# Performance work log

Hardware: AMD Instinct MI355X
Metric: run time of the kernel (lower is better)

## Reference

```python
import jax, jax.numpy as jnp
import numpy as np
import math

D_MODEL = 1024
NHEADS = 16
HEAD_DIM = D_MODEL // NHEADS
SEQLEN = 2048
BS = 4


def setup_inputs() -> dict:
    key = jax.random.key(0)
    kq, kk, kv, kwq, kwk, kwv, kwo = jax.random.split(key, 7)
    q = jax.random.normal(kq, (SEQLEN, BS, D_MODEL), dtype=jnp.float32)
    k = jax.random.normal(kk, (SEQLEN, BS, D_MODEL), dtype=jnp.float32)
    v = jax.random.normal(kv, (SEQLEN, BS, D_MODEL), dtype=jnp.float32)
    # proper RoPE table: (seq, head_dim//2, 2) with (cos, sin)
    inv_freq = 1.0 / (10000.0 ** (np.arange(0, HEAD_DIM, 2, dtype=np.float32) / HEAD_DIM))
    angles = np.arange(SEQLEN, dtype=np.float32)[:, None] * inv_freq[None, :]
    freqs_cis = jnp.asarray(np.stack([np.cos(angles), np.sin(angles)], axis=-1))
    scale = 1.0 / math.sqrt(D_MODEL)
    wq = jax.random.normal(kwq, (D_MODEL, D_MODEL), dtype=jnp.float32) * scale
    wk = jax.random.normal(kwk, (D_MODEL, D_MODEL), dtype=jnp.float32) * scale
    wv = jax.random.normal(kwv, (D_MODEL, D_MODEL), dtype=jnp.float32) * scale
    wo = jax.random.normal(kwo, (D_MODEL, D_MODEL), dtype=jnp.float32) * scale
    return {"q": q, "k": k, "v": v, "freqs_cis": freqs_cis,
            "wq": wq, "wk": wk, "wv": wv, "wo": wo}


def _apply_rope(x, fc):
    # x: (L, B, H, hd) -> complex rotation on (hd//2, 2) pairs
    L, B, H, hd = x.shape
    x2 = x.reshape(L, B, H, hd // 2, 2)
    fc = fc[:L].reshape(L, 1, 1, hd // 2, 2)  # broadcast over batch, heads
    real = x2[..., 0] * fc[..., 0] - x2[..., 1] * fc[..., 1]
    imag = x2[..., 1] * fc[..., 0] + x2[..., 0] * fc[..., 1]
    return jnp.stack([real, imag], axis=-1).reshape(L, B, H, hd)


def reference(q, k, v, freqs_cis, wq, wk, wv, wo):
    S, B, D = q.shape
    L = k.shape[0]
    H, hd = NHEADS, HEAD_DIM
    # torch Linear: y = x @ W^T, W: (out, in)
    xq = jnp.einsum('sbd,ed->sbe', q, wq).reshape(S, B, H, hd)
    xk = jnp.einsum('lbd,ed->lbe', k, wk).reshape(L, B, H, hd)
    xv = jnp.einsum('lbd,ed->lbe', v, wv).reshape(L, B, H, hd)
    xq = _apply_rope(xq, freqs_cis)
    xk = _apply_rope(xk, freqs_cis)
    # scores: (B, H, S, L)
    scores = jnp.einsum('sbhd,lbhd->bhsl', xq, xk) / math.sqrt(hd)
    probs = jax.nn.softmax(scores.astype(jnp.float32), axis=-1).astype(xq.dtype)
    out = jnp.einsum('bhsl,lbhd->sbhd', probs, xv).reshape(S, B, H * hd)
    return jnp.einsum('sbe,de->sbd', out, wo)
```

## Files before the change

### kernel.cpp

```cpp
#include <hip/hip_runtime.h>
#include <hip/hip_bf16.h>

#define S_LEN   2048
#define BATCH   4
#define DMODEL  1024
#define NHEADS  16
#define HDIM    64
#define MROWS   (S_LEN * BATCH)

#define NE_ 8388608u
#define WE_ 1048576u

typedef unsigned int uint32;
typedef __attribute__((ext_vector_type(8))) short bf16x8;
typedef __attribute__((ext_vector_type(4))) float f32x4;

__device__ __forceinline__ ushort f2bf(float f) {
    uint32 u = __float_as_uint(f);
    uint32 r = (u + 0x7FFFu + ((u >> 16) & 1u)) >> 16;
    return (ushort)r;
}

__device__ __forceinline__ uint32 pk_bf16(float a, float b) {
    uint32 r;
    asm("v_cvt_pk_bf16_f32 %0, %1, %2" : "=v"(r) : "v"(a), "v"(b));
    return r;
}

__device__ __forceinline__ float exp2_asm(float x) {
    float r;
    asm("v_exp_f32 %0, %1" : "=v"(r) : "v"(x));
    return r;
}

__device__ __forceinline__ void gl16(const ushort* g, ushort* l) {
    __builtin_amdgcn_global_load_lds(
        (const __attribute__((address_space(1))) unsigned int*)g,
        (__attribute__((address_space(3))) unsigned int*)l,
        16, 0, 0);
}

__global__ __launch_bounds__(256) void cvt_all(const float* __restrict__ q,
                                               const float* __restrict__ k,
                                               const float* __restrict__ v,
                                               const float* __restrict__ wq,
                                               const float* __restrict__ wk,
                                               const float* __restrict__ wv,
                                               const float* __restrict__ wo,
                                               ushort* __restrict__ ws) {
    int i = blockIdx.x * 256 + threadIdx.x;
    const float* src;
    ushort* dst;
    int j;
    if (i < 3 * 2097152) {
        int t = i >> 21;
        j = i & 2097151;
        src = (t == 0) ? q : (t == 1) ? k : v;
        dst = ws + (size_t)t * NE_;
    } else {
        int u2 = i - 3 * 2097152;
        int t = u2 >> 18;
        j = u2 & 262143;
        src = (t == 0) ? wq : (t == 1) ? wk : (t == 2) ? wv : wo;
        dst = ws + 3 * (size_t)NE_ + (size_t)t * WE_;
    }
    float4 f = ((const float4*)src)[j];
    ushort4 u;
    u.x = f2bf(f.x); u.y = f2bf(f.y); u.z = f2bf(f.z); u.w = f2bf(f.w);
    ((ushort4*)dst)[j] = u;
}

__global__ __launch_bounds__(256) void qk_gemm(const ushort* __restrict__ qb,
                                               const ushort* __restrict__ kb,
                                               const ushort* __restrict__ wqb,
                                               const ushort* __restrict__ wkb,
                                               const float* __restrict__ FC,
                                               ushort* __restrict__ Qh,
                                               ushort* __restrict__ Kh) {
    __shared__ __align__(16) ushort A_lds[128 * 32];
    __shared__ __align__(16) ushort B_lds[128 * 32];

    const int tid  = threadIdx.x;
    const int lane = tid & 63;
    const int wvx  = tid >> 6;
    const int wm   = wvx >> 1, wn = wvx & 1;
    const int quad = lane >> 4, l16 = lane & 15;
    const int pid   = blockIdx.x >> 9;
    const int local = blockIdx.x & 511;
    const int m0 = (local >> 3) * 128;
    const int n0 = (local & 7) * 128;

    const ushort* A = pid ? kb : qb;
    const ushort* W = pid ? wkb : wqb;
    ushort* outb    = pid ? Kh : Qh;
    const float osc = pid ? 1.0f : 0.18033688011111793f;

    const int srow = tid >> 2;
    const int scol = (tid & 3) * 8;

    f32x4 acc[4][4] = {};

    for (int k0 = 0; k0 < 1024; k0 += 32) {
        __syncthreads();
        gl16(&A[(size_t)(m0 + srow) * 1024 + k0 + scol],      &A_lds[tid * 8]);
        gl16(&A[(size_t)(m0 + 64 + srow) * 1024 + k0 + scol], &A_lds[2048 + tid * 8]);
        gl16(&W[(size_t)(n0 + srow) * 1024 + k0 + scol],      &B_lds[tid * 8]);
        gl16(&W[(size_t)(n0 + 64 + srow) * 1024 + k0 + scol], &B_lds[2048 + tid * 8]);
        __syncthreads();

        const ushort* Ab = &A_lds[(wm * 64 + l16) * 32 + quad * 8];
        const ushort* Bb = &B_lds[(wn * 64 + l16) * 32 + quad * 8];
        bf16x8 af[4], bfr[4];
#pragma unroll
        for (int i = 0; i < 4; ++i) af[i]  = *(const bf16x8*)(Ab + i * 512);
#pragma unroll
        for (int i = 0; i < 4; ++i) bfr[i] = *(const bf16x8*)(Bb + i * 512);
#pragma unroll
        for (int im = 0; im < 4; ++im)
#pragma unroll
            for (int in = 0; in < 4; ++in)
                acc[im][in] = __builtin_amdgcn_mfma_f32_16x16x32_bf16(
                    af[im], bfr[in], acc[im][in], 0, 0, 0);
    }

#pragma unroll
    for (int im = 0; im < 4; ++im) {
        int mbase = m0 + wm * 64 + im * 16 + quad * 4;
        int s = mbase >> 2;
#pragma unroll
        for (int in = 0; in < 4; ++in) {
            int e = n0 + wn * 64 + in * 16 + l16;
            int h = e >> 6, dd = e & 63;
            float2 cs = *(const float2*)&FC[s * 64 + (dd & ~1)];
            float sgn = (dd & 1) ? 1.0f : -1.0f;
#pragma unroll
            for (int rr = 0; rr < 4; ++rr) {
                float vv = acc[im][in][rr];
                float pp = __shfl_xor(vv, 1, 64);
                float ov = (vv * cs.x + sgn * pp * cs.y) * osc;
                outb[((size_t)(rr * NHEADS + h) * S_LEN + s) * HDIM + dd] = f2bf(ov);
            }
        }
    }
}

__global__ __launch_bounds__(256) void v_gemm(const ushort* __restrict__ vb,
                                              const ushort* __restrict__ wvb,
                                              ushort* __restrict__ Vt) {
    __shared__ __align__(16) ushort A_lds[128 * 32];
    __shared__ __align__(16) ushort B_lds[128 * 32];

    const int tid  = threadIdx.x;
    const int lane = tid & 63;
    const int wvx  = tid >> 6;
    const int wm   = wvx >> 1, wn = wvx & 1;
    const int quad = lane >> 4, l16 = lane & 15;
    const int m0 = (blockIdx.x >> 3) * 128;
    const int n0 = (blockIdx.x & 7) * 128;

    const int srow = tid >> 2;
    const int scol = (tid & 3) * 8;

    f32x4 acc[4][4] = {};

    for (int k0 = 0; k0 < 1024; k0 += 32) {
        __syncthreads();
        gl16(&vb[(size_t)(m0 + srow) * 1024 + k0 + scol],      &A_lds[tid * 8]);
        gl16(&vb[(size_t)(m0 + 64 + srow) * 1024 + k0 + scol], &A_lds[2048 + tid * 8]);
        gl16(&wvb[(size_t)(n0 + srow) * 1024 + k0 + scol],      &B_lds[tid * 8]);
        gl16(&wvb[(size_t)(n0 + 64 + srow) * 1024 + k0 + scol], &B_lds[2048 + tid * 8]);
        __syncthreads();

        const ushort* Ab = &A_lds[(wm * 64 + l16) * 32 + quad * 8];
        const ushort* Bb = &B_lds[(wn * 64 + l16) * 32 + quad * 8];
        bf16x8 af[4], bfr[4];
#pragma unroll
        for (int i = 0; i < 4; ++i) af[i]  = *(const bf16x8*)(Ab + i * 512);
#pragma unroll
        for (int i = 0; i < 4; ++i) bfr[i] = *(const bf16x8*)(Bb + i * 512);
#pragma unroll
        for (int im = 0; im < 4; ++im)
#pragma unroll
            for (int in = 0; in < 4; ++in)
                acc[im][in] = __builtin_amdgcn_mfma_f32_16x16x32_bf16(
                    af[im], bfr[in], acc[im][in], 0, 0, 0);
    }

#pragma unroll
    for (int im = 0; im < 4; ++im) {
        int mbase = m0 + wm * 64 + im * 16 + quad * 4;
        int s = mbase >> 2;
        int nt2 = (s >> 4) & 3;
        int qd  = (s >> 2) & 3;
        int r2  = s & 3;
        int pos = (s & ~63) | ((nt2 >> 1) << 5) | (qd << 3) | ((nt2 & 1) << 2) | r2;
#pragma unroll
        for (int in = 0; in < 4; ++in) {
            int e = n0 + wn * 64 + in * 16 + l16;
            int h = e >> 6, dd = e & 63;
#pragma unroll
            for (int rr = 0; rr < 4; ++rr) {
                Vt[((size_t)(rr * NHEADS + h) * HDIM + dd) * S_LEN + pos] =
                    f2bf(acc[im][in][rr]);
            }
        }
    }
}

__global__ __launch_bounds__(256) void out_gemm(const ushort* __restrict__ A,
                                                const ushort* __restrict__ W,
                                                float* __restrict__ outf) {
    __shared__ __align__(16) ushort A_lds[128 * 32];
    __shared__ __align__(16) ushort B_lds[128 * 32];

    const int tid  = threadIdx.x;
    const int lane = tid & 63;
    const int wvx  = tid >> 6;
    const int wm   = wvx >> 1, wn = wvx & 1;
    const int quad = lane >> 4, l16 = lane & 15;
    const int m0 = (blockIdx.x >> 3) * 128;
    const int n0 = (blockIdx.x & 7) * 128;

    const int srow = tid >> 2;
    const int scol = (tid & 3) * 8;

    f32x4 acc[4][4] = {};

    for (int k0 = 0; k0 < 1024; k0 += 32) {
        __syncthreads();
        gl16(&A[(size_t)(m0 + srow) * 1024 + k0 + scol],      &A_lds[tid * 8]);
        gl16(&A[(size_t)(m0 + 64 + srow) * 1024 + k0 + scol], &A_lds[2048 + tid * 8]);
        gl16(&W[(size_t)(n0 + srow) * 1024 + k0 + scol],      &B_lds[tid * 8]);
        gl16(&W[(size_t)(n0 + 64 + srow) * 1024 + k0 + scol], &B_lds[2048 + tid * 8]);
        __syncthreads();

        const ushort* Ab = &A_lds[(wm * 64 + l16) * 32 + quad * 8];
        const ushort* Bb = &B_lds[(wn * 64 + l16) * 32 + quad * 8];
        bf16x8 af[4], bfr[4];
#pragma unroll
        for (int i = 0; i < 4; ++i) af[i]  = *(const bf16x8*)(Ab + i * 512);
#pragma unroll
        for (int i = 0; i < 4; ++i) bfr[i] = *(const bf16x8*)(Bb + i * 512);
#pragma unroll
        for (int im = 0; im < 4; ++im)
#pragma unroll
            for (int in = 0; in < 4; ++in)
                acc[im][in] = __builtin_amdgcn_mfma_f32_16x16x32_bf16(
                    af[im], bfr[in], acc[im][in], 0, 0, 0);
    }

#pragma unroll
    for (int im = 0; im < 4; ++im) {
        int mbase = m0 + wm * 64 + im * 16 + quad * 4;
#pragma unroll
        for (int in = 0; in < 4; ++in) {
            int e = n0 + wn * 64 + in * 16 + l16;
#pragma unroll
            for (int rr = 0; rr < 4; ++rr)
                outf[(size_t)(mbase + rr) * 1024 + e] = acc[im][in][rr];
        }
    }
}

__global__ __launch_bounds__(256) void attn_mfma(const ushort* __restrict__ Qb,
                                                 const ushort* __restrict__ Kb,
                                                 const ushort* __restrict__ Vt,
                                                 ushort* __restrict__ Ob) {
    __shared__ __align__(16) ushort KV[8192];

    const int tid  = threadIdx.x;
    const int lane = tid & 63;
    const int wv   = tid >> 6;
    const int quad = lane >> 4;
    const int l16  = lane & 15;
    const int head = blockIdx.x >> 4;
    const int qt   = blockIdx.x & 15;
    const int q0   = qt * 128 + wv * 32;
    const size_t hb = (size_t)head * (S_LEN * HDIM);

    bf16x8 qf[2][2];
#pragma unroll
    for (int im = 0; im < 2; ++im)
#pragma unroll
        for (int kk = 0; kk < 2; ++kk)
            qf[im][kk] = *(const bf16x8*)
                &Qb[hb + (size_t)(q0 + im * 16 + l16) * HDIM + kk * 32 + quad * 8];

    f32x4 o[2][4] = {};
    float lsum[2] = {0.f, 0.f};

    const int srow = tid >> 3;
    const int scol = (((tid & 7) ^ (srow & 7)) * 8);
    const int sx   = (l16 & 7) * 8;

    for (int kc = 0; kc < S_LEN; kc += 64) {
        __syncthreads();
        gl16(&Kb[hb + (size_t)(kc + srow) * HDIM + scol],      &KV[tid * 8]);
        gl16(&Kb[hb + (size_t)(kc + 32 + srow) * HDIM + scol], &KV[2048 + tid * 8]);
        gl16(&Vt[hb + (size_t)srow * S_LEN + kc + scol],        &KV[4096 + tid * 8]);
        gl16(&Vt[hb + (size_t)(32 + srow) * S_LEN + kc + scol], &KV[4096 + 2048 + tid * 8]);
        __syncthreads();

        f32x4 st[2][4] = {};
#pragma unroll
        for (int nt = 0; nt < 4; ++nt) {
            bf16x8 kf0 = *(const bf16x8*)&KV[(nt * 16 + l16) * 64 + ((quad * 8) ^ sx)];
            bf16x8 kf1 = *(const bf16x8*)&KV[(nt * 16 + l16) * 64 + ((32 + quad * 8) ^ sx)];
#pragma unroll
            for (int im = 0; im < 2; ++im) {
                st[im][nt] = __builtin_amdgcn_mfma_f32_16x16x32_bf16(
                    kf0, qf[im][0], st[im][nt], 0, 0, 0);
                st[im][nt] = __builtin_amdgcn_mfma_f32_16x16x32_bf16(
                    kf1, qf[im][1], st[im][nt], 0, 0, 0);
            }
        }

        union { uint32 d[16]; bf16x8 v[4]; } P;
#pragma unroll
        for (int im = 0; im < 2; ++im) {
            float ls = 0.f;
#pragma unroll
            for (int nt = 0; nt < 4; ++nt) {
                float p0 = exp2_asm(st[im][nt][0]);
                float p1 = exp2_asm(st[im][nt][1]);
                float p2 = exp2_asm(st[im][nt][2]);
                float p3 = exp2_asm(st[im][nt][3]);
                ls += (p0 + p1) + (p2 + p3);
                P.d[im * 8 + nt * 2]     = pk_bf16(p0, p1);
                P.d[im * 8 + nt * 2 + 1] = pk_bf16(p2, p3);
            }
            lsum[im] += ls;
        }

#pragma unroll
        for (int dt = 0; dt < 4; ++dt) {
            bf16x8 vf0 = *(const bf16x8*)&KV[4096 + (dt * 16 + l16) * 64 + ((quad * 8) ^ sx)];
            bf16x8 vf1 = *(const bf16x8*)&KV[4096 + (dt * 16 + l16) * 64 + ((32 + quad * 8) ^ sx)];
#pragma unroll
            for (int im = 0; im < 2; ++im) {
                o[im][dt] = __builtin_amdgcn_mfma_f32_16x16x32_bf16(
                    vf0, P.v[im * 2], o[im][dt], 0, 0, 0);
                o[im][dt] = __builtin_amdgcn_mfma_f32_16x16x32_bf16(
                    vf1, P.v[im * 2 + 1], o[im][dt], 0, 0, 0);
            }
        }
    }

#pragma unroll
    for (int im = 0; im < 2; ++im) {
        lsum[im] += __shfl_xor(lsum[im], 16, 64);
        lsum[im] += __shfl_xor(lsum[im], 32, 64);
    }

    __syncthreads();
    ushort* Est = &KV[wv * 2048];
#pragma unroll
    for (int im = 0; im < 2; ++im) {
        float inv = 1.0f / lsum[im];
#pragma unroll
        for (int dt = 0; dt < 4; ++dt) {
            uint2 w;
            w.x = pk_bf16(o[im][dt][0] * inv, o[im][dt][1] * inv);
            w.y = pk_bf16(o[im][dt][2] * inv, o[im][dt][3] * inv);
            *(uint2*)&Est[(im * 16 + l16) * 64 + dt * 16 + quad * 4] = w;
        }
    }
    __syncthreads();

    const int row  = lane >> 1, half = lane & 1;
    const int b = head >> 4, h = head & 15;
    const size_t ob = (size_t)((q0 + row) * BATCH + b) * 1024 + h * 64 + half * 32;
#pragma unroll
    for (int e = 0; e < 4; ++e) {
        bf16x8 t = *(const bf16x8*)&Est[row * 64 + half * 32 + e * 8];
        *(bf16x8*)&Ob[ob + e * 8] = t;
    }
}

extern "C" void kernel_launch(void* const* d_in, const int* in_sizes, int n_in,
                              void* d_out, int out_size, void* d_ws, size_t ws_size,
                              hipStream_t stream) {
    const float* q   = (const float*)d_in[0];
    const float* k   = (const float*)d_in[1];
    const float* v   = (const float*)d_in[2];
    const float* fc  = (const float*)d_in[3];
    const float* wq  = (const float*)d_in[4];
    const float* wk  = (const float*)d_in[5];
    const float* wvp = (const float*)d_in[6];
    const float* wo  = (const float*)d_in[7];

    ushort* ws = (ushort*)d_ws;
    ushort* qb  = ws;
    ushort* kb  = ws + NE_;
    ushort* vb  = ws + 2 * (size_t)NE_;
    ushort* wqb = ws + 3 * (size_t)NE_;
    ushort* wkb = wqb + WE_;
    ushort* wvb = wqb + 2 * (size_t)WE_;
    ushort* wob = wqb + 3 * (size_t)WE_;

    ushort* Qh = (ushort*)d_out;
    ushort* Kh = Qh + NE_;
    ushort* Vt = ws;
    ushort* R3 = ws + NE_;

    cvt_all<<<28672, 256, 0, stream>>>(q, k, v, wq, wk, wvp, wo, ws);

    qk_gemm<<<1024, 256, 0, stream>>>(qb, kb, wqb, wkb, fc, Qh, Kh);

    v_gemm<<<512, 256, 0, stream>>>(vb, wvb, Vt);

    attn_mfma<<<1024, 256, 0, stream>>>(Qh, Kh, Vt, R3);

    out_gemm<<<512, 256, 0, stream>>>(R3, wob, (float*)d_out);
}
```

Measured before the change: 378.0 us.

## Double-buffer K/V tiles in attention with 128-key prefetch and MFMA priority

The attention kernel now loads K and V in 128-key tiles into two LDS buffers, prefetching the next tile while the current one is computed. This removes one of the two barriers per step and hides global-load latency behind the MFMA work. The MFMA sections are also wrapped in s_setprio to favour matrix issue. In exchange, LDS per block grows from 16 KB to 64 KB, which can lower occupancy and reduce latency hiding across blocks.

```diff
diff --git a/kernel.cpp b/kernel.cpp
--- a/kernel.cpp
+++ b/kernel.cpp
@@ -266,7 +266,7 @@
                                                  const ushort* __restrict__ Kb,
                                                  const ushort* __restrict__ Vt,
                                                  ushort* __restrict__ Ob) {
-    __shared__ __align__(16) ushort KV[8192];
+    __shared__ __align__(16) ushort KV[32768];
 
     const int tid  = threadIdx.x;
     const int lane = tid & 63;
@@ -293,57 +293,89 @@
     const int scol = (((tid & 7) ^ (srow & 7)) * 8);
     const int sx   = (l16 & 7) * 8;
 
-    for (int kc = 0; kc < S_LEN; kc += 64) {
-        __syncthreads();
-        gl16(&Kb[hb + (size_t)(kc + srow) * HDIM + scol],      &KV[tid * 8]);
-        gl16(&Kb[hb + (size_t)(kc + 32 + srow) * HDIM + scol], &KV[2048 + tid * 8]);
-        gl16(&Vt[hb + (size_t)srow * S_LEN + kc + scol],        &KV[4096 + tid * 8]);
-        gl16(&Vt[hb + (size_t)(32 + srow) * S_LEN + kc + scol], &KV[4096 + 2048 + tid * 8]);
-        __syncthreads();
-
-        f32x4 st[2][4] = {};
-#pragma unroll
-        for (int nt = 0; nt < 4; ++nt) {
-            bf16x8 kf0 = *(const bf16x8*)&KV[(nt * 16 + l16) * 64 + ((quad * 8) ^ sx)];
-            bf16x8 kf1 = *(const bf16x8*)&KV[(nt * 16 + l16) * 64 + ((32 + quad * 8) ^ sx)];
+    {
+        ushort* dst = &KV[0];
+        gl16(&Kb[hb + (size_t)(srow) * HDIM + scol],           dst + tid * 8);
+        gl16(&Kb[hb + (size_t)(32 + srow) * HDIM + scol],      dst + 2048 + tid * 8);
+        gl16(&Kb[hb + (size_t)(64 + srow) * HDIM + scol],      dst + 4096 + tid * 8);
+        gl16(&Kb[hb + (size_t)(96 + srow) * HDIM + scol],      dst + 6144 + tid * 8);
+        gl16(&Vt[hb + (size_t)srow * S_LEN + scol],            dst + 8192 + tid * 8);
+        gl16(&Vt[hb + (size_t)(32 + srow) * S_LEN + scol],     dst + 10240 + tid * 8);
+        gl16(&Vt[hb + (size_t)srow * S_LEN + 64 + scol],       dst + 12288 + tid * 8);
+        gl16(&Vt[hb + (size_t)(32 + srow) * S_LEN + 64 + scol], dst + 14336 + tid * 8);
+    }
+    __syncthreads();
+
+#pragma unroll 2
+    for (int t = 0; t < 16; ++t) {
+        if (t < 15) {
+            ushort* dst = &KV[((t + 1) & 1) * 16384];
+            const int kc = (t + 1) * 128;
+            gl16(&Kb[hb + (size_t)(kc + srow) * HDIM + scol],      dst + tid * 8);
+            gl16(&Kb[hb + (size_t)(kc + 32 + srow) * HDIM + scol], dst + 2048 + tid * 8);
+            gl16(&Kb[hb + (size_t)(kc + 64 + srow) * HDIM + scol], dst + 4096 + tid * 8);
+            gl16(&Kb[hb + (size_t)(kc + 96 + srow) * HDIM + scol], dst + 6144 + tid * 8);
+            gl16(&Vt[hb + (size_t)srow * S_LEN + kc + scol],            dst + 8192 + tid * 8);
+            gl16(&Vt[hb + (size_t)(32 + srow) * S_LEN + kc + scol],     dst + 10240 + tid * 8);
+            gl16(&Vt[hb + (size_t)srow * S_LEN + kc + 64 + scol],       dst + 12288 + tid * 8);
+            gl16(&Vt[hb + (size_t)(32 + srow) * S_LEN + kc + 64 + scol], dst + 14336 + tid * 8);
+        }
+
+        const ushort* cb = &KV[(t & 1) * 16384];
+#pragma unroll
+        for (int sp = 0; sp < 2; ++sp) {
+            const ushort* Ksub = cb + sp * 4096;
+            const ushort* Vsub = cb + 8192 + sp * 4096;
+
+            f32x4 st[2][4] = {};
+            __builtin_amdgcn_s_setprio(1);
+#pragma unroll
+            for (int nt = 0; nt < 4; ++nt) {
+                bf16x8 kf0 = *(const bf16x8*)&Ksub[(nt * 16 + l16) * 64 + ((quad * 8) ^ sx)];
+                bf16x8 kf1 = *(const bf16x8*)&Ksub[(nt * 16 + l16) * 64 + ((32 + quad * 8) ^ sx)];
+#pragma unroll
+                for (int im = 0; im < 2; ++im) {
+                    st[im][nt] = __builtin_amdgcn_mfma_f32_16x16x32_bf16(
+                        kf0, qf[im][0], st[im][nt], 0, 0, 0);
+                    st[im][nt] = __builtin_amdgcn_mfma_f32_16x16x32_bf16(
+                        kf1, qf[im][1], st[im][nt], 0, 0, 0);
+                }
+            }
+            __builtin_amdgcn_s_setprio(0);
+
+            union { uint32 d[16]; bf16x8 v[4]; } P;
 #pragma unroll
             for (int im = 0; im < 2; ++im) {
-                st[im][nt] = __builtin_amdgcn_mfma_f32_16x16x32_bf16(
-                    kf0, qf[im][0], st[im][nt], 0, 0, 0);
-                st[im][nt] = __builtin_amdgcn_mfma_f32_16x16x32_bf16(
-                    kf1, qf[im][1], st[im][nt], 0, 0, 0);
+                float ls = 0.f;
+#pragma unroll
+                for (int nt = 0; nt < 4; ++nt) {
+                    float p0 = exp2_asm(st[im][nt][0]);
+                    float p1 = exp2_asm(st[im][nt][1]);
+                    float p2 = exp2_asm(st[im][nt][2]);
+                    float p3 = exp2_asm(st[im][nt][3]);
+                    ls += (p0 + p1) + (p2 + p3);
+                    P.d[im * 8 + nt * 2]     = pk_bf16(p0, p1);
+                    P.d[im * 8 + nt * 2 + 1] = pk_bf16(p2, p3);
+                }
+                lsum[im] += ls;
             }
-        }
-
-        union { uint32 d[16]; bf16x8 v[4]; } P;
-#pragma unroll
-        for (int im = 0; im < 2; ++im) {
-            float ls = 0.f;
-#pragma unroll
-            for (int nt = 0; nt < 4; ++nt) {
-                float p0 = exp2_asm(st[im][nt][0]);
-                float p1 = exp2_asm(st[im][nt][1]);
-                float p2 = exp2_asm(st[im][nt][2]);
-                float p3 = exp2_asm(st[im][nt][3]);
-                ls += (p0 + p1) + (p2 + p3);
-                P.d[im * 8 + nt * 2]     = pk_bf16(p0, p1);
-                P.d[im * 8 + nt * 2 + 1] = pk_bf16(p2, p3);
+
+            __builtin_amdgcn_s_setprio(1);
+#pragma unroll
+            for (int dt = 0; dt < 4; ++dt) {
+                bf16x8 vf0 = *(const bf16x8*)&Vsub[(dt * 16 + l16) * 64 + ((quad * 8) ^ sx)];
+                bf16x8 vf1 = *(const bf16x8*)&Vsub[(dt * 16 + l16) * 64 + ((32 + quad * 8) ^ sx)];
+#pragma unroll
+                for (int im = 0; im < 2; ++im) {
+                    o[im][dt] = __builtin_amdgcn_mfma_f32_16x16x32_bf16(
+                        vf0, P.v[im * 2], o[im][dt], 0, 0, 0);
+                    o[im][dt] = __builtin_amdgcn_mfma_f32_16x16x32_bf16(
+                        vf1, P.v[im * 2 + 1], o[im][dt], 0, 0, 0);
+                }
             }
-            lsum[im] += ls;
-        }
-
-#pragma unroll
-        for (int dt = 0; dt < 4; ++dt) {
-            bf16x8 vf0 = *(const bf16x8*)&KV[4096 + (dt * 16 + l16) * 64 + ((quad * 8) ^ sx)];
-            bf16x8 vf1 = *(const bf16x8*)&KV[4096 + (dt * 16 + l16) * 64 + ((32 + quad * 8) ^ sx)];
-#pragma unroll
-            for (int im = 0; im < 2; ++im) {
-                o[im][dt] = __builtin_amdgcn_mfma_f32_16x16x32_bf16(
-                    vf0, P.v[im * 2], o[im][dt], 0, 0, 0);
-                o[im][dt] = __builtin_amdgcn_mfma_f32_16x16x32_bf16(
-                    vf1, P.v[im * 2 + 1], o[im][dt], 0, 0, 0);
-            }
-        }
+            __builtin_amdgcn_s_setprio(0);
+        }
+        __syncthreads();
     }
 
 #pragma unroll
@@ -352,7 +384,6 @@
         lsum[im] += __shfl_xor(lsum[im], 32, 64);
     }
 
-    __syncthreads();
     ushort* Est = &KV[wv * 2048];
 #pragma unroll
     for (int im = 0; im < 2; ++im) {
```

Result: faster. 364.8 us (-3.5%).
